# Kernel tuning notes

Hardware: AMD Instinct MI355X
Metric: run time of the kernel (lower is better)

Reference implementation:

```python
import jax, jax.numpy as jnp
import numpy as np

N, E = 4096, 131072
IN, HID, OUT = 128, 128, 256
H4, C4 = 4, HID            # first/middle GAT: 4 heads of 128 -> concat 512
CAT = H4 * C4              # 512
NH, DK = 8, OUT // 8       # dense MHA
EPS_LN = 1e-5


def setup_inputs() -> dict:
    key = jax.random.key(0)
    ks = jax.random.split(key, 32)
    s = 0.05
    inp = {
        "x": jax.random.normal(ks[0], (N, IN), jnp.float32),
        "edge_index": jax.random.randint(ks[1], (2, E), 0, N, jnp.int64),
        # GAT layer 0: in=128, heads=4, out=128
        "W0": jax.random.normal(ks[2], (IN, H4 * C4)) * s,
        "as0": jax.random.normal(ks[3], (H4, C4)) * s,
        "ad0": jax.random.normal(ks[4], (H4, C4)) * s,
        "b0": jnp.zeros((H4 * C4,)),
        # GAT layer 1: in=512, heads=4, out=128
        "W1": jax.random.normal(ks[5], (CAT, H4 * C4)) * s,
        "as1": jax.random.normal(ks[6], (H4, C4)) * s,
        "ad1": jax.random.normal(ks[7], (H4, C4)) * s,
        "b1": jnp.zeros((H4 * C4,)),
        # GAT layer 2: in=512, heads=1, out=256
        "W2": jax.random.normal(ks[8], (CAT, OUT)) * s,
        "as2": jax.random.normal(ks[9], (1, OUT)) * s,
        "ad2": jax.random.normal(ks[10], (1, OUT)) * s,
        "b2": jnp.zeros((OUT,)),
        # LayerNorms
        "g0": jnp.ones((CAT,)), "be0": jnp.zeros((CAT,)),
        "g1": jnp.ones((CAT,)), "be1": jnp.zeros((CAT,)),
        "g2": jnp.ones((OUT,)), "be2": jnp.zeros((OUT,)),
        # dense MHA on output_dim=256
        "wq": jax.random.normal(ks[11], (OUT, OUT)) * s, "bq": jnp.zeros((OUT,)),
        "wk": jax.random.normal(ks[12], (OUT, OUT)) * s, "bk": jnp.zeros((OUT,)),
        "wv": jax.random.normal(ks[13], (OUT, OUT)) * s, "bv": jnp.zeros((OUT,)),
        "wo": jax.random.normal(ks[14], (OUT, OUT)) * s, "bo": jnp.zeros((OUT,)),
    }
    return inp


def _layer_norm(x, g, b):
    mu = x.mean(-1, keepdims=True)
    var = ((x - mu) ** 2).mean(-1, keepdims=True)
    return (x - mu) * jax.lax.rsqrt(var + EPS_LN) * g + b


def _gat(x, src, dst, W, a_src, a_dst, bias, heads, out_c):
    # PyG GATConv (concat=True, negative_slope=0.2, self-loops pre-added)
    n = x.shape[0]
    xl = (x @ W).reshape(n, heads, out_c)            # [N,H,C]
    al_s = (xl * a_src).sum(-1)                      # [N,H]
    al_d = (xl * a_dst).sum(-1)                      # [N,H]
    alpha = jax.nn.leaky_relu(al_s[src] + al_d[dst], 0.2)  # [Etot,H]
    m = jax.ops.segment_max(alpha, dst, num_segments=n)
    e = jnp.exp(alpha - m[dst])
    denom = jax.ops.segment_sum(e, dst, num_segments=n)
    w = e / (denom[dst] + 1e-16)                     # [Etot,H]
    msg = w[:, :, None] * xl[src]                    # [Etot,H,C]
    out = jax.ops.segment_sum(msg, dst, num_segments=n)
    return out.reshape(n, heads * out_c) + bias


def _mha(x, wq, bq, wk, bk, wv, bv, wo, bo):
    # x: [1,N,D], 8 heads
    B, S, D = x.shape
    def split(y):
        return y.reshape(B, S, NH, DK).transpose(0, 2, 1, 3)
    Q, K, V = split(x @ wq + bq), split(x @ wk + bk), split(x @ wv + bv)
    scores = jnp.einsum('bhqd,bhkd->bhqk', Q, K) / np.sqrt(DK)
    attn = jax.nn.softmax(scores, axis=-1)
    out = jnp.einsum('bhqk,bhkd->bhqd', attn, V)
    out = out.transpose(0, 2, 1, 3).reshape(B, S, D)
    return out @ wo + bo


def reference(x, edge_index, W0, as0, ad0, b0, W1, as1, ad1, b1, W2, as2, ad2, b2,
              g0, be0, g1, be1, g2, be2, wq, bq, wk, bk, wv, bv, wo, bo):
    n = x.shape[0]
    loops = jnp.arange(n, dtype=edge_index.dtype)
    src = jnp.concatenate([edge_index[0], loops])
    dst = jnp.concatenate([edge_index[1], loops])

    # layer 0: in=128 -> 512; residual None (128 != 512)
    h = jax.nn.elu(_gat(x, src, dst, W0, as0, ad0, b0, H4, C4))
    h = _layer_norm(h, g0, be0)

    # layer 1: 512 -> 512; residual applies
    res = h
    h = jax.nn.elu(_gat(h, src, dst, W1, as1, ad1, b1, H4, C4))
    h = _layer_norm(h, g1, be1)
    h = h + res

    # layer 2: 512 -> 256, 1 head
    h = _gat(h, src, dst, W2, as2, ad2, b2, 1, OUT)
    h = _layer_norm(h, g2, be2)

    # dense self-attention over all nodes as one sequence
    h = _mha(h[None], wq, bq, wk, bk, wv, bv, wo, bo)[0]
    return h
```

## Files before the change

### kernel.cpp

```cpp
#include <hip/hip_runtime.h>
#include <math.h>

typedef __attribute__((ext_vector_type(8))) short short8;
typedef __attribute__((ext_vector_type(4))) float float4v;

#define QS 0.2550354f

#if __has_builtin(__builtin_amdgcn_exp2f)
#define EXP2(x) __builtin_amdgcn_exp2f(x)
#else
#define EXP2(x) __expf((x)*0.6931471805599453f)
#endif

__device__ __forceinline__ float waveReduceSum(float v){
  #pragma unroll
  for(int o=32;o>0;o>>=1) v += __shfl_down(v,o,64);
  return v;
}

__device__ __forceinline__ unsigned short f2bf(float f){
  unsigned int u = __float_as_uint(f);
  return (unsigned short)((u + 0x7FFFu + ((u>>16)&1u)) >> 16);
}
__device__ __forceinline__ float bf2f(unsigned short u){
  return __uint_as_float(((unsigned int)u)<<16);
}

__global__ __launch_bounds__(256) void prep(const float* __restrict__ x, unsigned short* __restrict__ xb,
                     const float* __restrict__ W0, unsigned short* __restrict__ W0t,
                     const float* __restrict__ W1, unsigned short* __restrict__ W1t,
                     const float* __restrict__ W2, unsigned short* __restrict__ W2t,
                     const float* __restrict__ wq, const float* __restrict__ wk,
                     const float* __restrict__ wv, unsigned short* __restrict__ wqkvt,
                     const float* __restrict__ bq, const float* __restrict__ bk,
                     const float* __restrict__ bv, float* __restrict__ bqkv,
                     const float* __restrict__ wo, unsigned short* __restrict__ wot,
                     const float* __restrict__ as0, const float* __restrict__ ad0, unsigned short* __restrict__ S0,
                     const float* __restrict__ as1, const float* __restrict__ ad1, unsigned short* __restrict__ S1,
                     const float* __restrict__ as2, const float* __restrict__ ad2, unsigned short* __restrict__ S2,
                     const int* __restrict__ ei, int E, int Etot, int* __restrict__ hist){
  int b = blockIdx.x, t = threadIdx.x;
  if(b < 2048){ int i = b*256 + t; xb[i] = f2bf(x[i]); return; }
  if(b == 2048){ bqkv[t] = bq[t]*QS; bqkv[256+t] = bk[t]; bqkv[512+t] = bv[t]; return; }
  if(b < 2225){
    __shared__ unsigned short tile[64][65];
    int tb = b - 2049;
    const float* src; unsigned short* dst; int K,N,roff,local; float sc = 1.f;
    if(tb<16){src=W0;dst=W0t;K=128;N=512;local=tb;roff=0;}
    else if(tb<80){src=W1;dst=W1t;K=512;N=512;local=tb-16;roff=0;}
    else if(tb<112){src=W2;dst=W2t;K=512;N=256;local=tb-80;roff=0;}
    else if(tb<128){src=wq;dst=wqkvt;K=256;N=256;local=tb-112;roff=0;sc=QS;}
    else if(tb<144){src=wk;dst=wqkvt;K=256;N=256;local=tb-128;roff=256;}
    else if(tb<160){src=wv;dst=wqkvt;K=256;N=256;local=tb-144;roff=512;}
    else {src=wo;dst=wot;K=256;N=256;local=tb-160;roff=0;}
    int ntiles = N>>6;
    int k0 = (local/ntiles)*64, n0 = (local%ntiles)*64;
    int r4 = t>>4, c4 = (t&15)*4;
    #pragma unroll
    for(int it=0;it<4;it++){
      int row = r4 + it*16;
      float4 v = *(const float4*)(src + (size_t)(k0+row)*N + n0 + c4);
      tile[row][c4+0]=f2bf(v.x*sc);
      tile[row][c4+1]=f2bf(v.y*sc);
      tile[row][c4+2]=f2bf(v.z*sc);
      tile[row][c4+3]=f2bf(v.w*sc);
    }
    __syncthreads();
    int r8 = t>>3, c8 = (t&7)*8;
    #pragma unroll
    for(int it=0;it<2;it++){
      int n = r8 + it*32;
      short8 o;
      #pragma unroll
      for(int j=0;j<8;j++) o[j] = (short)tile[c8+j][n];
      *(short8*)(dst + (size_t)(n0+n+roff)*K + k0 + c8) = o;
    }
    return;
  }
  if(b >= 3377){
    int e = (b-3377)*256 + t;
    if(e < Etot){
      int d = (e<E) ? (ei[E+e]&4095) : (e-E);
      atomicAdd(&hist[d], 1);
    }
    return;
  }
  int bb = b - 2225;
  const float *W,*as,*ad; unsigned short* S; int K,C,H,k;
  if(bb<128){W=W0;as=as0;ad=ad0;S=S0;K=128;C=128;H=4;k=bb;}
  else if(bb<640){W=W1;as=as1;ad=ad1;S=S1;K=512;C=128;H=4;k=bb-128;}
  else {W=W2;as=as2;ad=ad2;S=S2;K=512;C=256;H=1;k=bb-640;}
  int D = H*C;
  __shared__ float s1[4], s2[4];
  int lane=t&63, wid=t>>6;
  for(int h=0;h<H;h++){
    float ps=0.f, pd=0.f;
    for(int c=t;c<C;c+=256){
      float wv2 = W[k*D + h*C + c];
      ps += wv2*as[h*C+c];
      pd += wv2*ad[h*C+c];
    }
    ps = waveReduceSum(ps); pd = waveReduceSum(pd);
    if(lane==0){ s1[wid]=ps; s2[wid]=pd; }
    __syncthreads();
    if(t==0){
      float u=s1[0]+s1[1]+s1[2]+s1[3], v=s2[0]+s2[1]+s2[2]+s2[3];
      S[h*K+k]=f2bf(u); S[(4+h)*K+k]=f2bf(v);
    }
    __syncthreads();
  }
  if(t==0){
    for(int h=H;h<4;h++){ S[h*K+k]=0; S[(4+h)*K+k]=0; }
    for(int r=8;r<16;r++) S[r*K+k]=0;
  }
}

__global__ __launch_bounds__(256) void gemm_mfma(const unsigned short* __restrict__ A,
                                                 const unsigned short* __restrict__ Bt,
                                                 const float* __restrict__ bias,
                                                 float* __restrict__ C,
                                                 unsigned short* __restrict__ Cb,
                                                 unsigned short* __restrict__ VtT,
                                                 const unsigned short* __restrict__ Wsd,
                                                 float* __restrict__ als,
                                                 float* __restrict__ ald,
                                                 int M, int K, int N){
  int t = threadIdx.x, lane = t & 63, w = t >> 6;
  int m = lane & 15, g = lane >> 4;
  int bm = blockIdx.y * 64, bn = blockIdx.x * 64;

  __shared__ unsigned short As[2][64*72];
  __shared__ unsigned short Bs[2][64*72];

  int sr = t >> 3;
  int sc = (t & 7) * 8;
  const unsigned short* Ap = A  + (bm + sr)*K + sc;
  const unsigned short* Bp = Bt + (bn + sr)*K + sc;
  bool doC = (Wsd != nullptr) && (blockIdx.x == 0);

  float4v acc[4];
  #pragma unroll
  for(int nt=0;nt<4;nt++) acc[nt] = (float4v){0.f,0.f,0.f,0.f};
  float4v acc2 = (float4v){0.f,0.f,0.f,0.f};

  short8 a0 = *(const short8*)(Ap);
  short8 a1 = *(const short8*)(Ap + 32*K);
  short8 b0 = *(const short8*)(Bp);
  short8 b1 = *(const short8*)(Bp + 32*K);

  int buf = 0;
  for(int k0=0;k0<K;k0+=64){
    *(short8*)&As[buf][sr*72 + sc]      = a0;
    *(short8*)&As[buf][(sr+32)*72 + sc] = a1;
    *(short8*)&Bs[buf][sr*72 + sc]      = b0;
    *(short8*)&Bs[buf][(sr+32)*72 + sc] = b1;
    if(k0+64 < K){
      a0 = *(const short8*)(Ap + k0+64);
      a1 = *(const short8*)(Ap + 32*K + k0+64);
      b0 = *(const short8*)(Bp + k0+64);
      b1 = *(const short8*)(Bp + 32*K + k0+64);
    }
    __syncthreads();

    #pragma unroll
    for(int ks=0;ks<2;ks++){
      short8 aA = *(const short8*)&As[buf][(w*16 + m)*72 + ks*32 + g*8];
      #pragma unroll
      for(int nt=0;nt<4;nt++){
        short8 bB = *(const short8*)&Bs[buf][(nt*16 + m)*72 + ks*32 + g*8];
        acc[nt] = __builtin_amdgcn_mfma_f32_16x16x32_bf16(aA, bB, acc[nt], 0,0,0);
      }
      if(doC){
        short8 bW = *(const short8*)(Wsd + m*K + k0 + ks*32 + g*8);
        acc2 = __builtin_amdgcn_mfma_f32_16x16x32_bf16(aA, bW, acc2, 0,0,0);
      }
    }
    buf ^= 1;
  }

  if(VtT && bn >= 512){
    __syncthreads();
    unsigned short* T = &As[0][0];
    #pragma unroll
    for(int nt=0;nt<4;nt++){
      int col = bn + nt*16 + m;
      float bv = bias ? bias[col] : 0.f;
      unsigned int r0 = __float_as_uint(acc[nt][0]+bv) + 0x8000u;
      unsigned int r1 = __float_as_uint(acc[nt][1]+bv) + 0x8000u;
      unsigned int r2 = __float_as_uint(acc[nt][2]+bv) + 0x8000u;
      unsigned int r3 = __float_as_uint(acc[nt][3]+bv) + 0x8000u;
      uint2 pk;
      pk.x = __builtin_amdgcn_perm(r1, r0, 0x07060302u);
      pk.y = __builtin_amdgcn_perm(r3, r2, 0x07060302u);
      *(uint2*)&T[(nt*16 + m)*72 + w*16 + g*4] = pk;
    }
    __syncthreads();
    int d  = t >> 2;
    int qc = (t & 3) * 16;
    short8 v0 = *(const short8*)&T[d*72 + qc];
    short8 v1 = *(const short8*)&T[d*72 + qc + 8];
    unsigned short* dst = VtT + (size_t)(bn - 512 + d)*M + bm + qc;
    *(short8*)(dst)     = v0;
    *(short8*)(dst + 8) = v1;
    return;
  }

  #pragma unroll
  for(int nt=0;nt<4;nt++){
    int col = bn + nt*16 + m;
    float bv = bias ? bias[col] : 0.f;
    #pragma unroll
    for(int r=0;r<4;r++){
      int row = bm + w*16 + g*4 + r;
      float v = acc[nt][r] + bv;
      if(C)  C[row*N + col]  = v;
      if(Cb) Cb[row*N + col] = f2bf(v);
    }
  }
  if(doC){
    #pragma unroll
    for(int r=0;r<4;r++){
      int row = bm + w*16 + g*4 + r;
      if(m<4)      als[row*4 + m]     = acc2[r];
      else if(m<8) ald[row*4 + (m-4)] = acc2[r];
    }
  }
}

__global__ __launch_bounds__(1024) void csr_scan(const int* __restrict__ hist,
                                                 int* __restrict__ row_ptr,
                                                 int* __restrict__ wcnt, int N){
  __shared__ int sh[1024];
  int t = threadIdx.x;
  int base[4];
  int s = 0;
  #pragma unroll
  for(int i=0;i<4;i++){ base[i]=s; s += hist[t*4+i]; }
  sh[t] = s;
  __syncthreads();
  for(int off=1; off<1024; off<<=1){
    int x = (t>=off) ? sh[t-off] : 0;
    __syncthreads();
    sh[t] += x;
    __syncthreads();
  }
  int excl = (t==0) ? 0 : sh[t-1];
  #pragma unroll
  for(int i=0;i<4;i++){
    row_ptr[t*4+i] = excl + base[i];
    wcnt[t*4+i]    = excl + base[i];
  }
  if(t==1023) row_ptr[N] = excl + s;
}

__global__ void csr_scatter(const int* __restrict__ ei, int E, int Etot,
                            int* __restrict__ wcnt, int* __restrict__ col){
  int e = blockIdx.x*256 + threadIdx.x;
  if(e>=Etot) return;
  int s,d;
  if(e<E){ s=ei[e]&4095; d=ei[E+e]&4095; } else { s=d=e-E; }
  int pos = atomicAdd(&wcnt[d], 1);
  col[pos] = s;
}

#define CE 128
__global__ void gat_gather_ln(const int* __restrict__ rp,
                              const int* __restrict__ col,
                              const unsigned short* __restrict__ xlb,
                              const float* __restrict__ als,
                              const float* __restrict__ ald,
                              const float* __restrict__ bias,
                              const float* __restrict__ gw,
                              const float* __restrict__ be,
                              const float* __restrict__ res,
                              float* __restrict__ out,
                              unsigned short* __restrict__ outb,
                              int D, int logC, int do_elu){
  int n = blockIdx.x, t = threadIdx.x;
  int c0 = t*2;
  int h = c0 >> logC;
  int rowW = D >> 1;
  float4 advv = *(const float4*)(ald + n*4);
  int start = rp[n], end = rp[n+1];
  const unsigned int* xw = (const unsigned int*)xlb;

  __shared__ float pw[2][CE*4];
  __shared__ int offs[2][CE];

  float acc0=0.f, acc1=0.f, den=0.f;
  int nch = (end - start + CE - 1) / CE;

  {
    int cnt = min(CE, end-start);
    if(t < cnt){
      int s = col[start+t];
      offs[0][t] = s*rowW;
      float4 av = *(const float4*)(als + s*4);
      #pragma unroll
      for(int hh=0;hh<4;hh++){
        float a = ((const float*)&av)[hh] + ((const float*)&advv)[hh];
        a = a>0.f ? a : 0.2f*a;
        pw[0][t*4+hh] = __expf(a);
      }
    }
  }

  for(int c=0;c<nch;c++){
    __syncthreads();
    if(c+1 < nch){
      int base = start + (c+1)*CE;
      int cnt = min(CE, end-base);
      int b2 = (c+1)&1;
      if(t < cnt){
        int s = col[base+t];
        offs[b2][t] = s*rowW;
        float4 av = *(const float4*)(als + s*4);
        #pragma unroll
        for(int hh=0;hh<4;hh++){
          float a = ((const float*)&av)[hh] + ((const float*)&advv)[hh];
          a = a>0.f ? a : 0.2f*a;
          pw[b2][t*4+hh] = __expf(a);
        }
      }
    }
    int base = start + c*CE;
    int cnt = min(CE, end-base);
    int b = c&1;
    #pragma unroll 8
    for(int j=0;j<cnt;j++){
      float p = pw[b][j*4+h];
      unsigned int u = xw[offs[b][j] + t];
      acc0 += p * bf2f((unsigned short)(u & 0xffffu));
      acc1 += p * bf2f((unsigned short)(u >> 16));
      den += p;
    }
  }

  float inv_d = 1.f/(den + 1e-16f);
  float v0 = acc0*inv_d + bias[c0];
  float v1 = acc1*inv_d + bias[c0+1];
  if(do_elu){
    v0 = v0>0.f ? v0 : expm1f(v0);
    v1 = v1>0.f ? v1 : expm1f(v1);
  }
  __shared__ float sh[4];
  int lane=t&63, wid=t>>6, nw = blockDim.x>>6;
  float sum = waveReduceSum(v0+v1);
  if(lane==0) sh[wid]=sum;
  __syncthreads();
  float mean = 0.f;
  for(int i=0;i<nw;i++) mean += sh[i];
  mean /= (float)D;
  __syncthreads();
  float d0 = v0-mean, d1 = v1-mean;
  float vs = waveReduceSum(d0*d0 + d1*d1);
  if(lane==0) sh[wid]=vs;
  __syncthreads();
  float var = 0.f;
  for(int i=0;i<nw;i++) var += sh[i];
  var /= (float)D;
  float inv = rsqrtf(var + 1e-5f);
  float y0 = d0*inv*gw[c0]   + be[c0];
  float y1 = d1*inv*gw[c0+1] + be[c0+1];
  if(res){ float2 rv = *(const float2*)(res + n*D + c0); y0 += rv.x; y1 += rv.y; }
  if(out) *(float2*)(out + n*D + c0) = make_float2(y0, y1);
  if(outb) ((unsigned int*)outb)[n*rowW + t] =
      (unsigned int)f2bf(y0) | ((unsigned int)f2bf(y1) << 16);
}

#define KS 8
__global__ __launch_bounds__(256) void attention12(const unsigned short* __restrict__ QKV,
                                                   const unsigned short* __restrict__ Vt,
                                                   float* __restrict__ Op,
                                                   float* __restrict__ lp, int S){
  const int RS = 768;
  int qb = blockIdx.x * 64;
  int h  = blockIdx.y;
  int ks = blockIdx.z;
  int t  = threadIdx.x;
  int lane = t & 63, w = t >> 6;
  int m = lane & 15, g = lane >> 4;
  int m7 = m & 7;

  __shared__ unsigned short Ps[64*64];
  __shared__ unsigned short Vs[32*64];
  __shared__ unsigned short Ks[64*36];

  short8 aQ = *(const short8*)(QKV + (qb + w*16 + m)*RS + h*32 + g*8);
  short8 vones;
  #pragma unroll
  for(int j=0;j<8;j++) vones[j] = (short)0x3F80;

  float4v o0 = {0.f,0.f,0.f,0.f}, o1 = {0.f,0.f,0.f,0.f};
  float4v lacc = {0.f,0.f,0.f,0.f};

  int r8 = t>>3, c8 = t&7;
  int kr = t>>2, kc = (t&3)*8;
  int kA = ks*(S/KS), kB = kA + S/KS;

  for(int kt=kA; kt<kB; kt+=64){
    short8 v = *(const short8*)(Vt + (h*32 + r8)*S + kt + c8*8);
    short8 kv = *(const short8*)(QKV + (kt + kr)*RS + 256 + h*32 + kc);
    __syncthreads();
    *(short8*)&Vs[r8*64 + ((c8 ^ (r8&7))<<3)] = v;
    *(short8*)&Ks[kr*36 + kc] = kv;
    __syncthreads();

    #pragma unroll
    for(int nt=0;nt<4;nt++){
      short8 aK = *(const short8*)&Ks[(nt*16 + m)*36 + g*8];
      float4v acc = {0.f,0.f,0.f,0.f};
      acc = __builtin_amdgcn_mfma_f32_16x16x32_bf16(aK, aQ, acc, 0,0,0);
      float p0 = EXP2(acc[0]);
      float p1 = EXP2(acc[1]);
      float p2 = EXP2(acc[2]);
      float p3 = EXP2(acc[3]);
      unsigned int r0 = __float_as_uint(p0) + 0x8000u;
      unsigned int r1 = __float_as_uint(p1) + 0x8000u;
      unsigned int r2 = __float_as_uint(p2) + 0x8000u;
      unsigned int r3 = __float_as_uint(p3) + 0x8000u;
      uint2 pk;
      pk.x = __builtin_amdgcn_perm(r1, r0, 0x07060302u);
      pk.y = __builtin_amdgcn_perm(r3, r2, 0x07060302u);
      *(uint2*)&Ps[(w*16 + m)*64 + (((2*nt + (g>>1)) ^ m7)<<3) + ((g&1)<<2)] = pk;
    }

    #pragma unroll
    for(int kh=0;kh<2;kh++){
      int swz = ((kh*4 + g) ^ m7) << 3;
      short8 aP  = *(const short8*)&Ps[(w*16 + m)*64 + swz];
      short8 bV0 = *(const short8*)&Vs[m*64       + swz];
      short8 bV1 = *(const short8*)&Vs[(16+m)*64  + swz];
      o0 = __builtin_amdgcn_mfma_f32_16x16x32_bf16(aP, bV0, o0, 0,0,0);
      o1 = __builtin_amdgcn_mfma_f32_16x16x32_bf16(aP, bV1, o1, 0,0,0);
      lacc = __builtin_amdgcn_mfma_f32_16x16x32_bf16(aP, vones, lacc, 0,0,0);
    }
  }

  float* Ob = Op + (size_t)ks*S*256;
  #pragma unroll
  for(int r=0;r<4;r++){
    int q = qb + w*16 + g*4 + r;
    Ob[q*256 + h*32 + m]      = o0[r];
    Ob[q*256 + h*32 + 16 + m] = o1[r];
  }
  if(m==0){
    #pragma unroll
    for(int r=0;r<4;r++){
      int q = qb + w*16 + g*4 + r;
      lp[ks*S*8 + q*8 + h] = lacc[r];
    }
  }
}

__global__ __launch_bounds__(256) void combine(const float* __restrict__ Op,
                                               const float* __restrict__ lp,
                                               unsigned short* __restrict__ aob, int S){
  int q = blockIdx.x, t = threadIdx.x;
  int h = t >> 5;
  float o = 0.f, l = 0.f;
  #pragma unroll
  for(int s=0;s<KS;s++) o += Op[(size_t)s*S*256 + q*256 + t];
  #pragma unroll
  for(int s=0;s<KS;s++) l += lp[s*S*8 + q*8 + h];
  aob[q*256 + t] = f2bf(o / l);
}

extern "C" void kernel_launch(void* const* d_in, const int* in_sizes, int n_in,
                              void* d_out, int out_size, void* d_ws, size_t ws_size,
                              hipStream_t stream) {
  const float* x   = (const float*)d_in[0];
  const int*   ei  = (const int*)d_in[1];
  const float* W0  = (const float*)d_in[2];
  const float* as0 = (const float*)d_in[3];
  const float* ad0 = (const float*)d_in[4];
  const float* b0  = (const float*)d_in[5];
  const float* W1  = (const float*)d_in[6];
  const float* as1 = (const float*)d_in[7];
  const float* ad1 = (const float*)d_in[8];
  const float* b1  = (const float*)d_in[9];
  const float* W2  = (const float*)d_in[10];
  const float* as2 = (const float*)d_in[11];
  const float* ad2 = (const float*)d_in[12];
  const float* b2  = (const float*)d_in[13];
  const float* g0  = (const float*)d_in[14];
  const float* be0 = (const float*)d_in[15];
  const float* g1  = (const float*)d_in[16];
  const float* be1 = (const float*)d_in[17];
  const float* g2  = (const float*)d_in[18];
  const float* be2 = (const float*)d_in[19];
  const float* wq  = (const float*)d_in[20];
  const float* bq  = (const float*)d_in[21];
  const float* wk  = (const float*)d_in[22];
  const float* bk  = (const float*)d_in[23];
  const float* wv  = (const float*)d_in[24];
  const float* bv  = (const float*)d_in[25];
  const float* wo  = (const float*)d_in[26];
  const float* bo  = (const float*)d_in[27];
  float* out = (float*)d_out;

  const int N = 4096;
  const int E = in_sizes[1] / 2;
  const int Etot = E + N;

  char* p = (char*)d_ws;
  auto alloc = [&](size_t bytes){ char* r = p; p += (bytes + 255) & ~(size_t)255; return r; };

  float* h0   = (float*)alloc(N*512*4);
  float* als  = (float*)alloc(N*4*4);
  float* ald  = (float*)alloc(N*4*4);
  unsigned short* xb   = (unsigned short*)alloc(N*128*2);
  unsigned short* xlb  = (unsigned short*)alloc(N*512*2);
  unsigned short* h0b  = (unsigned short*)alloc(N*512*2);
  unsigned short* h1b  = (unsigned short*)alloc(N*512*2);
  unsigned short* h2b  = (unsigned short*)alloc(N*256*2);
  unsigned short* QKVb = (unsigned short*)alloc((size_t)N*768*2);
  unsigned short* Vt   = (unsigned short*)alloc(256*N*2);
  unsigned short* aob  = (unsigned short*)alloc(N*256*2);
  unsigned short* W0t  = (unsigned short*)alloc(512*128*2);
  unsigned short* W1t  = (unsigned short*)alloc(512*512*2);
  unsigned short* W2t  = (unsigned short*)alloc(256*512*2);
  unsigned short* wqkvt= (unsigned short*)alloc(768*256*2);
  float* bqkv = (float*)alloc(768*4);
  unsigned short* wot  = (unsigned short*)alloc(256*256*2);
  unsigned short* Wsd0 = (unsigned short*)alloc(16*128*2);
  unsigned short* Wsd1 = (unsigned short*)alloc(16*512*2);
  unsigned short* Wsd2 = (unsigned short*)alloc(16*512*2);
  float* Op = (float*)alloc((size_t)KS*N*256*4);
  float* lp = (float*)alloc((size_t)KS*N*8*4);
  int* hist = (int*)alloc(N*4);
  int* wcnt = (int*)alloc(N*4);
  int* rp   = (int*)alloc((N+2)*4);
  int* col  = (int*)alloc(Etot*4);

  hipMemsetAsync(hist, 0, N*sizeof(int), stream);
  prep<<<3377 + (Etot+255)/256, 256, 0, stream>>>(x, xb, W0, W0t, W1, W1t, W2, W2t,
                                 wq, wk, wv, wqkvt, bq, bk, bv, bqkv, wo, wot,
                                 as0, ad0, Wsd0, as1, ad1, Wsd1, as2, ad2, Wsd2,
                                 ei, E, Etot, hist);

  csr_scan<<<1, 1024, 0, stream>>>(hist, rp, wcnt, N);
  csr_scatter<<<(Etot+255)/256, 256, 0, stream>>>(ei, E, Etot, wcnt, col);

  gemm_mfma<<<dim3(8, 64), 256, 0, stream>>>(xb, W0t, nullptr, nullptr, xlb, nullptr, Wsd0, als, ald, N, 128, 512);
  gat_gather_ln<<<N, 256, 0, stream>>>(rp, col, xlb, als, ald, b0, g0, be0,
                                       nullptr, h0, h0b, 512, 7, 1);

  gemm_mfma<<<dim3(8, 64), 256, 0, stream>>>(h0b, W1t, nullptr, nullptr, xlb, nullptr, Wsd1, als, ald, N, 512, 512);
  gat_gather_ln<<<N, 256, 0, stream>>>(rp, col, xlb, als, ald, b1, g1, be1,
                                       h0, nullptr, h1b, 512, 7, 1);

  gemm_mfma<<<dim3(4, 64), 256, 0, stream>>>(h1b, W2t, nullptr, nullptr, xlb, nullptr, Wsd2, als, ald, N, 512, 256);
  gat_gather_ln<<<N, 128, 0, stream>>>(rp, col, xlb, als, ald, b2, g2, be2,
                                       nullptr, nullptr, h2b, 256, 8, 0);

  gemm_mfma<<<dim3(12, 64), 256, 0, stream>>>(h2b, wqkvt, bqkv, nullptr, QKVb, Vt, nullptr, nullptr, nullptr, N, 256, 768);
  attention12<<<dim3(N/64, 8, KS), 256, 0, stream>>>(QKVb, Vt, Op, lp, N);
  combine<<<N, 256, 0, stream>>>(Op, lp, aob, N);
  gemm_mfma<<<dim3(4, 64), 256, 0, stream>>>(aob, wot, bo, out, nullptr, nullptr, nullptr, nullptr, nullptr, N, 256, 256);
}
```

Baseline: 269.1 us.

## Vectorize x conversion, prefetch attention tiles, drop ones-MFMA, halve key splits

The x-to-bf16 conversion in prep now handles eight elements per thread with vector loads, cutting its block count from 2048 to 256. The attention kernel register-prefetches the next K/V tile while the current one is processed. It also replaces the extra MFMA against a ones vector with a scalar running sum plus cross-lane shuffles for the softmax denominator. The key-split factor drops from 8 to 4, which halves the partial-output traffic in combine but leaves fewer attention blocks in flight.

```diff
diff --git a/kernel.cpp b/kernel.cpp
--- a/kernel.cpp
+++ b/kernel.cpp
@@ -40,11 +40,20 @@
                      const float* __restrict__ as2, const float* __restrict__ ad2, unsigned short* __restrict__ S2,
                      const int* __restrict__ ei, int E, int Etot, int* __restrict__ hist){
   int b = blockIdx.x, t = threadIdx.x;
-  if(b < 2048){ int i = b*256 + t; xb[i] = f2bf(x[i]); return; }
-  if(b == 2048){ bqkv[t] = bq[t]*QS; bqkv[256+t] = bk[t]; bqkv[512+t] = bv[t]; return; }
-  if(b < 2225){
+  if(b < 256){
+    int i = (b*256 + t)*8;
+    float4 u0 = *(const float4*)(x + i);
+    float4 u1 = *(const float4*)(x + i + 4);
+    short8 o;
+    o[0]=(short)f2bf(u0.x); o[1]=(short)f2bf(u0.y); o[2]=(short)f2bf(u0.z); o[3]=(short)f2bf(u0.w);
+    o[4]=(short)f2bf(u1.x); o[5]=(short)f2bf(u1.y); o[6]=(short)f2bf(u1.z); o[7]=(short)f2bf(u1.w);
+    *(short8*)(xb + i) = o;
+    return;
+  }
+  if(b == 256){ bqkv[t] = bq[t]*QS; bqkv[256+t] = bk[t]; bqkv[512+t] = bv[t]; return; }
+  if(b < 433){
     __shared__ unsigned short tile[64][65];
-    int tb = b - 2049;
+    int tb = b - 257;
     const float* src; unsigned short* dst; int K,N,roff,local; float sc = 1.f;
     if(tb<16){src=W0;dst=W0t;K=128;N=512;local=tb;roff=0;}
     else if(tb<80){src=W1;dst=W1t;K=512;N=512;local=tb-16;roff=0;}
@@ -77,15 +86,15 @@
     }
     return;
   }
-  if(b >= 3377){
-    int e = (b-3377)*256 + t;
+  if(b >= 1585){
+    int e = (b-1585)*256 + t;
     if(e < Etot){
       int d = (e<E) ? (ei[E+e]&4095) : (e-E);
       atomicAdd(&hist[d], 1);
     }
     return;
   }
-  int bb = b - 2225;
+  int bb = b - 433;
   const float *W,*as,*ad; unsigned short* S; int K,C,H,k;
   if(bb<128){W=W0;as=as0;ad=ad0;S=S0;K=128;C=128;H=4;k=bb;}
   else if(bb<640){W=W1;as=as1;ad=ad1;S=S1;K=512;C=128;H=4;k=bb-128;}
@@ -368,7 +377,7 @@
       (unsigned int)f2bf(y0) | ((unsigned int)f2bf(y1) << 16);
 }
 
-#define KS 8
+#define KS 4
 __global__ __launch_bounds__(256) void attention12(const unsigned short* __restrict__ QKV,
                                                    const unsigned short* __restrict__ Vt,
                                                    float* __restrict__ Op,
@@ -387,23 +396,25 @@
   __shared__ unsigned short Ks[64*36];
 
   short8 aQ = *(const short8*)(QKV + (qb + w*16 + m)*RS + h*32 + g*8);
-  short8 vones;
-  #pragma unroll
-  for(int j=0;j<8;j++) vones[j] = (short)0x3F80;
 
   float4v o0 = {0.f,0.f,0.f,0.f}, o1 = {0.f,0.f,0.f,0.f};
-  float4v lacc = {0.f,0.f,0.f,0.f};
+  float den = 0.f;
 
   int r8 = t>>3, c8 = t&7;
   int kr = t>>2, kc = (t&3)*8;
   int kA = ks*(S/KS), kB = kA + S/KS;
 
+  short8 v  = *(const short8*)(Vt + (h*32 + r8)*S + kA + c8*8);
+  short8 kv = *(const short8*)(QKV + (kA + kr)*RS + 256 + h*32 + kc);
+
   for(int kt=kA; kt<kB; kt+=64){
-    short8 v = *(const short8*)(Vt + (h*32 + r8)*S + kt + c8*8);
-    short8 kv = *(const short8*)(QKV + (kt + kr)*RS + 256 + h*32 + kc);
     __syncthreads();
     *(short8*)&Vs[r8*64 + ((c8 ^ (r8&7))<<3)] = v;
     *(short8*)&Ks[kr*36 + kc] = kv;
+    if(kt+64 < kB){
+      v  = *(const short8*)(Vt + (h*32 + r8)*S + kt+64 + c8*8);
+      kv = *(const short8*)(QKV + (kt+64 + kr)*RS + 256 + h*32 + kc);
+    }
     __syncthreads();
 
     #pragma unroll
@@ -415,6 +426,7 @@
       float p1 = EXP2(acc[1]);
       float p2 = EXP2(acc[2]);
       float p3 = EXP2(acc[3]);
+      den += (p0+p1)+(p2+p3);
       unsigned int r0 = __float_as_uint(p0) + 0x8000u;
       unsigned int r1 = __float_as_uint(p1) + 0x8000u;
       unsigned int r2 = __float_as_uint(p2) + 0x8000u;
@@ -433,9 +445,11 @@
       short8 bV1 = *(const short8*)&Vs[(16+m)*64  + swz];
       o0 = __builtin_amdgcn_mfma_f32_16x16x32_bf16(aP, bV0, o0, 0,0,0);
       o1 = __builtin_amdgcn_mfma_f32_16x16x32_bf16(aP, bV1, o1, 0,0,0);
-      lacc = __builtin_amdgcn_mfma_f32_16x16x32_bf16(aP, vones, lacc, 0,0,0);
-    }
-  }
+    }
+  }
+
+  den += __shfl_xor(den, 16, 64);
+  den += __shfl_xor(den, 32, 64);
 
   float* Ob = Op + (size_t)ks*S*256;
   #pragma unroll
@@ -444,12 +458,9 @@
     Ob[q*256 + h*32 + m]      = o0[r];
     Ob[q*256 + h*32 + 16 + m] = o1[r];
   }
-  if(m==0){
-    #pragma unroll
-    for(int r=0;r<4;r++){
-      int q = qb + w*16 + g*4 + r;
-      lp[ks*S*8 + q*8 + h] = lacc[r];
-    }
+  if(g==0){
+    int q = qb + w*16 + m;
+    lp[ks*S*8 + q*8 + h] = den;
   }
 }
 
@@ -534,7 +545,7 @@
   int* col  = (int*)alloc(Etot*4);
 
   hipMemsetAsync(hist, 0, N*sizeof(int), stream);
-  prep<<<3377 + (Etot+255)/256, 256, 0, stream>>>(x, xb, W0, W0t, W1, W1t, W2, W2t,
+  prep<<<1585 + (Etot+255)/256, 256, 0, stream>>>(x, xb, W0, W0t, W1, W1t, W2, W2t,
                                  wq, wk, wv, wqkvt, bq, bk, bv, bqkv, wo, wot,
                                  as0, ad0, Wsd0, as1, ad1, Wsd1, as2, ad2, Wsd2,
                                  ei, E, Etot, hist);
```

New measurement: 268.1 us. Within noise of the previous version (-0.4%).
